# Performance work log

Hardware: AMD Instinct MI355X
Metric: run time of the kernel (lower is better)

Reference implementation:

```python
import jax, jax.numpy as jnp
import numpy as np

B, T, C, H = 4, 2048, 1024, 16
D = C // H  # head dim = 64


def _layernorm(x, g, b, eps=1e-5):
    mu = jnp.mean(x, axis=-1, keepdims=True)
    var = jnp.var(x, axis=-1, keepdims=True)
    return (x - mu) * jax.lax.rsqrt(var + eps) * g + b


def setup_inputs() -> dict:
    key = jax.random.key(0)
    ks = jax.random.split(key, 8)
    s = 0.02
    return {
        "x": jax.random.normal(ks[0], (B, T, C), dtype=jnp.float32),
        "ln1_g": jnp.ones((C,), jnp.float32),
        "ln1_b": jnp.zeros((C,), jnp.float32),
        "W_qkv": jax.random.normal(ks[1], (C, 3 * C), dtype=jnp.float32) * s,
        "b_qkv": jnp.zeros((3 * C,), jnp.float32),
        "W_o": jax.random.normal(ks[2], (C, C), dtype=jnp.float32) * s,
        "b_o": jnp.zeros((C,), jnp.float32),
        "ln2_g": jnp.ones((C,), jnp.float32),
        "ln2_b": jnp.zeros((C,), jnp.float32),
        "W_fc": jax.random.normal(ks[3], (C, 4 * C), dtype=jnp.float32) * s,
        "b_fc": jnp.zeros((4 * C,), jnp.float32),
        "W_pr": jax.random.normal(ks[4], (4 * C, C), dtype=jnp.float32) * s,
        "b_pr": jnp.zeros((C,), jnp.float32),
    }


def reference(x, ln1_g, ln1_b, W_qkv, b_qkv, W_o, b_o, ln2_g, ln2_b, W_fc, b_fc, W_pr, b_pr):
    # --- attention sub-block ---
    h = _layernorm(x, ln1_g, ln1_b)
    qkv = h @ W_qkv + b_qkv                       # [B,T,3C]
    q, k, v = jnp.split(qkv, 3, axis=-1)
    q = q.reshape(B, T, H, D).transpose(0, 2, 1, 3)  # [B,H,T,D]
    k = k.reshape(B, T, H, D).transpose(0, 2, 1, 3)
    v = v.reshape(B, T, H, D).transpose(0, 2, 1, 3)
    att = jnp.einsum("bhqd,bhkd->bhqk", q, k) * (1.0 / jnp.sqrt(jnp.float32(D)))
    causal = jnp.tril(jnp.ones((T, T), dtype=bool))
    att = jnp.where(causal, att, jnp.float32(-jnp.inf))
    att = jax.nn.softmax(att, axis=-1)
    y = jnp.einsum("bhqk,bhkd->bhqd", att, v)     # [B,H,T,D]
    y = y.transpose(0, 2, 1, 3).reshape(B, T, C)
    y = y @ W_o + b_o
    x = x + y
    # --- FFN sub-block ---
    h2 = _layernorm(x, ln2_g, ln2_b)
    f = jax.nn.gelu(h2 @ W_fc + b_fc, approximate=False)  # nn.GELU default = exact
    f = f @ W_pr + b_pr
    return x + f
```

## Files before the change

kernel.cpp:

```cpp
#include <hip/hip_runtime.h>
#include <math.h>

#define Bz 4
#define Tz 2048
#define Cz 1024
#define Hz 16
#define Dz 64
#define MTOK (Bz*Tz)

typedef __attribute__((ext_vector_type(8))) short short8;
typedef __attribute__((ext_vector_type(4))) short short4v;
typedef __attribute__((ext_vector_type(4))) float f32x4;

typedef unsigned int u32_g __attribute__((address_space(1)));
typedef unsigned int u32_l __attribute__((address_space(3)));

__device__ __forceinline__ unsigned short f2bf(float f) {
    unsigned int u = __float_as_uint(f);
    u += 0x7fffu + ((u >> 16) & 1u);
    return (unsigned short)(u >> 16);
}
__device__ __forceinline__ float bf2f(unsigned short h) {
    return __uint_as_float((unsigned int)h << 16);
}

__device__ __forceinline__ void async_cp16(const unsigned short* g, unsigned short* l) {
    __builtin_amdgcn_global_load_lds((const u32_g*)g, (u32_l*)l, 16, 0, 0);
}

__global__ void transpose_w(const float* __restrict__ W, unsigned short* __restrict__ Wt,
                            int K, int N) {
    __shared__ float tile[32][33];
    int n0 = blockIdx.x * 32, k0 = blockIdx.y * 32;
    int tx = threadIdx.x, ty = threadIdx.y;
    #pragma unroll
    for (int i = 0; i < 4; i++)
        tile[ty + i * 8][tx] = W[(size_t)(k0 + ty + i * 8) * N + n0 + tx];
    __syncthreads();
    #pragma unroll
    for (int i = 0; i < 4; i++)
        Wt[(size_t)(n0 + ty + i * 8) * K + k0 + tx] = f2bf(tile[tx][ty + i * 8]);
}

__global__ void ln_kernel(const float* __restrict__ x, const float* __restrict__ g,
                          const float* __restrict__ bb, unsigned short* __restrict__ out) {
    int tok = blockIdx.x, tid = threadIdx.x;
    const float4 v = ((const float4*)(x + (size_t)tok * Cz))[tid];
    float s = v.x + v.y + v.z + v.w;
    float sq = v.x * v.x + v.y * v.y + v.z * v.z + v.w * v.w;
    #pragma unroll
    for (int m = 1; m < 64; m <<= 1) { s += __shfl_xor(s, m); sq += __shfl_xor(sq, m); }
    __shared__ float red[8];
    int lane = tid & 63, wid = tid >> 6;
    if (!lane) { red[wid] = s; red[4 + wid] = sq; }
    __syncthreads();
    s = red[0] + red[1] + red[2] + red[3];
    sq = red[4] + red[5] + red[6] + red[7];
    float mu = s * (1.0f / Cz);
    float var = sq * (1.0f / Cz) - mu * mu;
    float rs = rsqrtf(var + 1e-5f);
    float4 gv = ((const float4*)g)[tid];
    float4 bv = ((const float4*)bb)[tid];
    short4v o;
    o[0] = f2bf((v.x - mu) * rs * gv.x + bv.x);
    o[1] = f2bf((v.y - mu) * rs * gv.y + bv.y);
    o[2] = f2bf((v.z - mu) * rs * gv.z + bv.z);
    o[3] = f2bf((v.w - mu) * rs * gv.w + bv.w);
    *(short4v*)(out + (size_t)tok * Cz + tid * 4) = o;
}

#define MODE_QKV 0
#define MODE_RESID 1
#define MODE_GELU 2

template <int MODE>
__launch_bounds__(256)
__global__ void gemm_bt(const unsigned short* __restrict__ A, const unsigned short* __restrict__ Bt,
                        int ld, int K, int N, const float* __restrict__ bias,
                        float* __restrict__ outf, unsigned short* __restrict__ outb,
                        const float* __restrict__ resid,
                        unsigned short* __restrict__ qo, unsigned short* __restrict__ ko,
                        unsigned short* __restrict__ vo) {
    __shared__ __align__(16) unsigned short As[128 * 64];
    __shared__ __align__(16) unsigned short Bs[128 * 64];
    const int tid = threadIdx.x;
    const int lane = tid & 63;
    const int quad = lane >> 4, l15 = lane & 15;
    const int wid = tid >> 6;
    const int id = blockIdx.x;
    const int m0 = ((id & 7) * 8 + ((id >> 3) & 7)) * 128;
    const int n0 = (id >> 6) * 128;
    const int wm = (wid >> 1) * 64, wn = (wid & 1) * 64;
    f32x4 acc[4][4] = {};

    const int srow = lane >> 3;
    const int scol = ((lane & 7) ^ srow) * 8;
    const unsigned short* Ag[4];
    const unsigned short* Bg[4];
    unsigned short* lA[4];
    unsigned short* lB[4];
    #pragma unroll
    for (int j = 0; j < 4; j++) {
        const int row = wid * 32 + j * 8 + srow;
        Ag[j] = A + (size_t)(m0 + row) * ld + scol;
        Bg[j] = Bt + (size_t)(n0 + row) * ld + scol;
        lA[j] = &As[(wid * 4 + j) * 512 + lane * 8];
        lB[j] = &Bs[(wid * 4 + j) * 512 + lane * 8];
    }

    for (int k0 = 0; k0 < K; k0 += 64) {
        #pragma unroll
        for (int j = 0; j < 4; j++) async_cp16(Ag[j] + k0, lA[j]);
        #pragma unroll
        for (int j = 0; j < 4; j++) async_cp16(Bg[j] + k0, lB[j]);
        __syncthreads();
        #pragma unroll
        for (int ks = 0; ks < 2; ks++) {
            short8 af[4], bfr[4];
            #pragma unroll
            for (int i = 0; i < 4; i++) {
                const int ra = wm + i * 16 + l15;
                af[i] = *(const short8*)&As[ra * 64 + (((ks << 2) + quad) ^ (ra & 7)) * 8];
            }
            #pragma unroll
            for (int i = 0; i < 4; i++) {
                const int rb = wn + i * 16 + l15;
                bfr[i] = *(const short8*)&Bs[rb * 64 + (((ks << 2) + quad) ^ (rb & 7)) * 8];
            }
            #pragma unroll
            for (int mi = 0; mi < 4; mi++)
                #pragma unroll
                for (int ni = 0; ni < 4; ni++)
                    acc[mi][ni] = __builtin_amdgcn_mfma_f32_16x16x32_bf16(af[mi], bfr[ni], acc[mi][ni], 0, 0, 0);
        }
        __syncthreads();
    }

    #pragma unroll
    for (int ni = 0; ni < 4; ni++) {
        const int col = n0 + wn + ni * 16 + l15;
        const float bv = bias[col];
        #pragma unroll
        for (int mi = 0; mi < 4; mi++) {
            #pragma unroll
            for (int r = 0; r < 4; r++) {
                const int row = m0 + wm + mi * 16 + quad * 4 + r;
                float val = acc[mi][ni][r] + bv;
                if constexpr (MODE == MODE_QKV) {
                    int which = col >> 10, cc = col & 1023;
                    int hh = cc >> 6, dd = cc & 63;
                    int b_ = row >> 11, t = row & 2047;
                    if (which == 2) {
                        vo[((size_t)(b_ * Hz + hh) * Dz + dd) * Tz + t] = f2bf(val);
                    } else {
                        unsigned short* dst = which ? ko : qo;
                        dst[((size_t)(b_ * Hz + hh) * Tz + t) * Dz + dd] = f2bf(val);
                    }
                } else if constexpr (MODE == MODE_RESID) {
                    size_t idx = (size_t)row * N + col;
                    outf[idx] = val + resid[idx];
                } else {
                    float c = val * (1.0f + 0.044715f * val * val);
                    float e = __expf(1.5957691216057308f * c);
                    float gz = val * e / (1.0f + e);
                    outb[(size_t)row * N + col] = f2bf(gz);
                }
            }
        }
    }
}

#define ATT_SC 0.18033688011112042f
__launch_bounds__(256)
__global__ void attn_kernel(const unsigned short* __restrict__ qb, const unsigned short* __restrict__ kb,
                            const unsigned short* __restrict__ vt, unsigned short* __restrict__ y) {
    __shared__ __align__(16) unsigned short Klds[64 * 64];
    __shared__ __align__(16) unsigned short Vtl[64 * 64];
    __shared__ __align__(16) unsigned short Plds[4][16 * 72];
    const int tid = threadIdx.x;
    const int lane = tid & 63, wid = tid >> 6;
    const int quad = lane >> 4, l15 = lane & 15;
    const int bh = blockIdx.x & 63;
    const int qt = 15 - (int)(blockIdx.x >> 6);
    const size_t baseT = (size_t)bh * Tz;
    const size_t vbase = (size_t)bh * Dz;
    const int qb0 = qt * 128;

    short8 qf[2][2];
    {
        const unsigned short* q0p = qb + (baseT + qb0 + wid * 16 + l15) * Dz + quad * 8;
        qf[0][0] = *(const short8*)q0p;
        qf[0][1] = *(const short8*)(q0p + 32);
        const unsigned short* q1p = q0p + (size_t)64 * Dz;
        qf[1][0] = *(const short8*)q1p;
        qf[1][1] = *(const short8*)(q1p + 32);
    }

    f32x4 o[2][4] = {};
    float lsum[2][4] = {{0.f,0.f,0.f,0.f},{0.f,0.f,0.f,0.f}};

    const int srow = lane >> 3;
    const int swz = ((lane & 7) ^ srow) * 8;
    const unsigned short* kg0 = kb + (baseT + wid * 8 + srow) * Dz + swz;
    const unsigned short* kg1 = kg0 + (size_t)32 * Dz;
    const unsigned short* vg0 = vt + (vbase + wid * 8 + srow) * Tz + swz;
    const unsigned short* vg1 = vg0 + (size_t)32 * Tz;
    unsigned short* kl0 = &Klds[wid * 512 + lane * 8];
    unsigned short* kl1 = kl0 + 2048;
    unsigned short* vl0 = &Vtl[wid * 512 + lane * 8];
    unsigned short* vl1 = vl0 + 2048;

    const int nchunk = 2 * qt + 2;

    for (int ci = 0; ci < nchunk; ci++) {
        const int k0 = ci * 64;
        async_cp16(kg0 + (size_t)k0 * Dz, kl0);
        async_cp16(kg1 + (size_t)k0 * Dz, kl1);
        async_cp16(vg0 + k0, vl0);
        async_cp16(vg1 + k0, vl1);
// ... 47 lines not shown
        __syncthreads();
    }

    const int b_ = bh >> 4, hh = bh & 15;
    #pragma unroll
    for (int t = 0; t < 2; t++)
        #pragma unroll
        for (int r = 0; r < 4; r++) {
            float ls = lsum[t][r];
            #pragma unroll
            for (int m = 1; m < 16; m <<= 1) ls += __shfl_xor(ls, m);
            float inv = 1.0f / ls;
            size_t tok = (size_t)qb0 + t * 64 + wid * 16 + quad * 4 + r;
            unsigned short* yr = y + ((size_t)b_ * Tz + tok) * Cz + hh * Dz;
            #pragma unroll
            for (int nc = 0; nc < 4; nc++)
                yr[nc * 16 + l15] = f2bf(o[t][nc][r] * inv);
        }
}

extern "C" void kernel_launch(void* const* d_in, const int* in_sizes, int n_in,
                              void* d_out, int out_size, void* d_ws, size_t ws_size,
                              hipStream_t stream) {
    const float* x    = (const float*)d_in[0];
    const float* ln1g = (const float*)d_in[1];
    const float* ln1b = (const float*)d_in[2];
    const float* Wqkv = (const float*)d_in[3];
    const float* bqkv = (const float*)d_in[4];
    const float* Wo   = (const float*)d_in[5];
    const float* bo   = (const float*)d_in[6];
    const float* ln2g = (const float*)d_in[7];
    const float* ln2b = (const float*)d_in[8];
    const float* Wfc  = (const float*)d_in[9];
    const float* bfc  = (const float*)d_in[10];
    const float* Wpr  = (const float*)d_in[11];
    const float* bpr  = (const float*)d_in[12];
    float* out = (float*)d_out;

    char* ws = (char*)d_ws;
    size_t off = 0;
    auto alloc = [&](size_t bytes) { void* p = ws + off; off += (bytes + 255) & ~(size_t)255; return p; };
    unsigned short* wqkv_t = (unsigned short*)alloc((size_t)3072 * 1024 * 2);
    unsigned short* wo_t   = (unsigned short*)alloc((size_t)1024 * 1024 * 2);
    unsigned short* wfc_t  = (unsigned short*)alloc((size_t)4096 * 1024 * 2);
    unsigned short* wpr_t  = (unsigned short*)alloc((size_t)1024 * 4096 * 2);
    unsigned short* h1     = (unsigned short*)alloc((size_t)MTOK * Cz * 2);
    unsigned short* qbuf   = (unsigned short*)alloc((size_t)MTOK * Cz * 2);
    unsigned short* kbuf   = (unsigned short*)alloc((size_t)MTOK * Cz * 2);
    unsigned short* vbuf   = (unsigned short*)alloc((size_t)MTOK * Cz * 2);
    unsigned short* ybuf   = (unsigned short*)alloc((size_t)MTOK * Cz * 2);
    float*          x1     = (float*)alloc((size_t)MTOK * Cz * 4);
    unsigned short* h2     = (unsigned short*)alloc((size_t)MTOK * Cz * 2);
    unsigned short* fbuf   = (unsigned short*)alloc((size_t)MTOK * 4096 * 2);

    dim3 tb(32, 8);
    transpose_w<<<dim3(3072 / 32, 1024 / 32), tb, 0, stream>>>(Wqkv, wqkv_t, 1024, 3072);
    transpose_w<<<dim3(1024 / 32, 1024 / 32), tb, 0, stream>>>(Wo, wo_t, 1024, 1024);
    transpose_w<<<dim3(4096 / 32, 1024 / 32), tb, 0, stream>>>(Wfc, wfc_t, 1024, 4096);
    transpose_w<<<dim3(1024 / 32, 4096 / 32), tb, 0, stream>>>(Wpr, wpr_t, 4096, 1024);

    ln_kernel<<<MTOK, 256, 0, stream>>>(x, ln1g, ln1b, h1);
    gemm_bt<MODE_QKV><<<64 * 24, 256, 0, stream>>>(h1, wqkv_t, 1024, 1024, 3072, bqkv,
                                                   nullptr, nullptr, nullptr, qbuf, kbuf, vbuf);
    attn_kernel<<<1024, 256, 0, stream>>>(qbuf, kbuf, vbuf, ybuf);
    gemm_bt<MODE_RESID><<<64 * 8, 256, 0, stream>>>(ybuf, wo_t, 1024, 1024, 1024, bo,
                                                    x1, nullptr, x, nullptr, nullptr, nullptr);
    ln_kernel<<<MTOK, 256, 0, stream>>>(x1, ln2g, ln2b, h2);
    gemm_bt<MODE_GELU><<<64 * 32, 256, 0, stream>>>(h2, wfc_t, 1024, 1024, 4096, bfc,
                                                    nullptr, fbuf, nullptr, nullptr, nullptr, nullptr);
    gemm_bt<MODE_RESID><<<64 * 8, 256, 0, stream>>>(fbuf, wpr_t, 4096, 4096, 1024, bpr,
                                                    out, nullptr, x1, nullptr, nullptr, nullptr);
}
```

Before: 530.6 us.

## Replace GEMMs with 8-wave 256-row tiles and double-buffered async LDS pipeline

Replaces the single-buffered 128x128 GEMM with two 512-thread kernels that use 256x256 or 256x128 tiles. Each K step is split into 32-wide halves, and the next tiles are prefetched with async global-to-LDS copies that overlap the MFMA work, synchronised by explicit vmcnt waits and barriers. It also adds s_setprio around the MFMA bursts. The larger tiles raise data reuse and cut LDS load overhead, but they need more registers (one block per CU) and give fewer blocks, so wave quantisation can get worse on the smaller GEMMs.

```diff
diff --git a/kernel.cpp b/kernel.cpp
--- a/kernel.cpp
+++ b/kernel.cpp
@@ -27,6 +27,10 @@
 __device__ __forceinline__ void async_cp16(const unsigned short* g, unsigned short* l) {
     __builtin_amdgcn_global_load_lds((const u32_g*)g, (u32_l*)l, 16, 0, 0);
 }
+
+#define BARX() __builtin_amdgcn_s_barrier()
+#define LGKM0() do { asm volatile("s_waitcnt lgkmcnt(0)" ::: "memory"); __builtin_amdgcn_sched_barrier(0); } while (0)
+#define VMC(n) asm volatile("s_waitcnt vmcnt(" #n ")" ::: "memory")
 
 __global__ void transpose_w(const float* __restrict__ W, unsigned short* __restrict__ Wt,
                             int K, int N) {
@@ -74,97 +78,228 @@
 #define MODE_GELU 2
 
 template <int MODE>
-__launch_bounds__(256)
-__global__ void gemm_bt(const unsigned short* __restrict__ A, const unsigned short* __restrict__ Bt,
-                        int ld, int K, int N, const float* __restrict__ bias,
-                        float* __restrict__ outf, unsigned short* __restrict__ outb,
-                        const float* __restrict__ resid,
-                        unsigned short* __restrict__ qo, unsigned short* __restrict__ ko,
-                        unsigned short* __restrict__ vo) {
-    __shared__ __align__(16) unsigned short As[128 * 64];
-    __shared__ __align__(16) unsigned short Bs[128 * 64];
+__device__ __forceinline__ void write_elem(int row, int col, float val, int N,
+                                           float* __restrict__ outf, unsigned short* __restrict__ outb,
+                                           const float* __restrict__ resid,
+                                           unsigned short* __restrict__ qo, unsigned short* __restrict__ ko,
+                                           unsigned short* __restrict__ vo) {
+    if constexpr (MODE == MODE_QKV) {
+        int which = col >> 10, cc = col & 1023;
+        int hh = cc >> 6, dd = cc & 63;
+        int b_ = row >> 11, t = row & 2047;
+        if (which == 2) {
+            vo[((size_t)(b_ * Hz + hh) * Dz + dd) * Tz + t] = f2bf(val);
+        } else {
+            unsigned short* dst = which ? ko : qo;
+            dst[((size_t)(b_ * Hz + hh) * Tz + t) * Dz + dd] = f2bf(val);
+        }
+    } else if constexpr (MODE == MODE_RESID) {
+        size_t idx = (size_t)row * N + col;
+        outf[idx] = val + resid[idx];
+    } else {
+        float c = val * (1.0f + 0.044715f * val * val);
+        float e = __expf(1.5957691216057308f * c);
+        outb[(size_t)row * N + col] = f2bf(val * e / (1.0f + e));
+    }
+}
+
+template <int MODE>
+__launch_bounds__(512, 1)
+__global__ void gemm8_n256(const unsigned short* __restrict__ A, const unsigned short* __restrict__ Bt,
+                           int lda, int K, int N, const float* __restrict__ bias,
+                           float* __restrict__ outf, unsigned short* __restrict__ outb,
+                           const float* __restrict__ resid,
+                           unsigned short* __restrict__ qo, unsigned short* __restrict__ ko,
+                           unsigned short* __restrict__ vo) {
+    __shared__ __align__(16) unsigned short As[2][2][256 * 32];
+    __shared__ __align__(16) unsigned short Bs[2][2][256 * 32];
     const int tid = threadIdx.x;
     const int lane = tid & 63;
+    const int wid = tid >> 6;
     const int quad = lane >> 4, l15 = lane & 15;
+    const int gm = wid >> 2, gn = wid & 3;
+    const int id = blockIdx.x;
+    const int rr = id >> 3;
+    const int m0 = ((id & 7) * 4 + (rr & 3)) * 256;
+    const int n0 = (rr >> 2) * 256;
+    const int NT = K >> 6;
+
+    const int srow = tid >> 2;
+    const int lseg = (tid & 3) ^ ((tid >> 3) & 3);
+    const unsigned short* Ag0 = A + (size_t)(m0 + srow) * lda + lseg * 8;
+    const unsigned short* Ag1 = A + (size_t)(m0 + 128 + srow) * lda + lseg * 8;
+    const unsigned short* Bg0 = Bt + (size_t)(n0 + srow) * lda + lseg * 8;
+    const unsigned short* Bg1 = Bt + (size_t)(n0 + 128 + srow) * lda + lseg * 8;
+
+    f32x4 acc[8][4] = {};
+    short8 af[8], bf[4];
+
+#define STA(bufd, kkd, tt) do { \
+    async_cp16(Ag0 + (size_t)(tt) * 64 + (kkd) * 32, &As[bufd][kkd][tid * 8]); \
+    async_cp16(Ag1 + (size_t)(tt) * 64 + (kkd) * 32, &As[bufd][kkd][4096 + tid * 8]); } while (0)
+#define STB(bufd, kkd, tt) do { \
+    async_cp16(Bg0 + (size_t)(tt) * 64 + (kkd) * 32, &Bs[bufd][kkd][tid * 8]); \
+    async_cp16(Bg1 + (size_t)(tt) * 64 + (kkd) * 32, &Bs[bufd][kkd][4096 + tid * 8]); } while (0)
+#define RDA(kkd) do { _Pragma("unroll") for (int mi = 0; mi < 8; mi++) { \
+    const int ra = gm * 128 + mi * 16 + l15; \
+    af[mi] = *(const short8*)&As[buf][kkd][ra * 32 + ((quad ^ ((ra >> 1) & 3)) << 3)]; } } while (0)
+#define RDB2(kkd, nia, nib) do { \
+    { const int rb = gn * 64 + (nia) * 16 + l15; \
+      bf[nia] = *(const short8*)&Bs[buf][kkd][rb * 32 + ((quad ^ ((rb >> 1) & 3)) << 3)]; } \
+    { const int rb = gn * 64 + (nib) * 16 + l15; \
+      bf[nib] = *(const short8*)&Bs[buf][kkd][rb * 32 + ((quad ^ ((rb >> 1) & 3)) << 3)]; } } while (0)
+#define MM2(nia, nib) do { _Pragma("unroll") for (int mi = 0; mi < 8; mi++) { \
+    acc[mi][nia] = __builtin_amdgcn_mfma_f32_16x16x32_bf16(af[mi], bf[nia], acc[mi][nia], 0, 0, 0); \
+    acc[mi][nib] = __builtin_amdgcn_mfma_f32_16x16x32_bf16(af[mi], bf[nib], acc[mi][nib], 0, 0, 0); } } while (0)
+
+    STA(0, 0, 0); STB(0, 0, 0);
+    STA(0, 1, 0); STB(0, 1, 0);
+    STA(1, 0, 1); STB(1, 0, 1);
+    VMC(8);
+    BARX();
+
+    for (int t = 0; t < NT; t++) {
+        const int buf = t & 1;
+        const int nb = buf ^ 1;
+        RDA(0); RDB2(0, 0, 1);
+        if (t + 1 < NT) STA(nb, 1, t + 1);
+        BARX(); LGKM0();
+        __builtin_amdgcn_s_setprio(1);
+        MM2(0, 1);
+        __builtin_amdgcn_s_setprio(0);
+        BARX();
+        RDB2(0, 2, 3);
+        if (t + 1 < NT) STB(nb, 1, t + 1);
+        BARX(); LGKM0();
+        __builtin_amdgcn_s_setprio(1);
+        MM2(2, 3);
+        __builtin_amdgcn_s_setprio(0);
+        if (t + 1 < NT) { VMC(8); } else { VMC(0); }
+        BARX();
+        RDA(1); RDB2(1, 0, 1);
+        if (t + 2 < NT) STA(buf, 0, t + 2);
+        BARX(); LGKM0();
+        __builtin_amdgcn_s_setprio(1);
+        MM2(0, 1);
+        __builtin_amdgcn_s_setprio(0);
+        BARX();
+        RDB2(1, 2, 3);
+        if (t + 2 < NT) STB(buf, 0, t + 2);
+        BARX(); LGKM0();
+        __builtin_amdgcn_s_setprio(1);
+        MM2(2, 3);
+        __builtin_amdgcn_s_setprio(0);
+        if (t + 2 < NT) { VMC(8); } else if (t + 1 < NT) { VMC(4); } else { VMC(0); }
+        BARX();
+    }
+#undef STA
+#undef STB
+#undef RDA
+#undef RDB2
+#undef MM2
+
+    #pragma unroll
+    for (int ni = 0; ni < 4; ni++) {
+        const int col = n0 + gn * 64 + ni * 16 + l15;
+        const float bv = bias[col];
+        #pragma unroll
+        for (int mi = 0; mi < 8; mi++) {
+            #pragma unroll
+            for (int r = 0; r < 4; r++) {
+                const int row = m0 + gm * 128 + mi * 16 + quad * 4 + r;
+                write_elem<MODE>(row, col, acc[mi][ni][r] + bv, N, outf, outb, resid, qo, ko, vo);
+            }
+        }
+    }
+}
+
+template <int MODE>
+__launch_bounds__(512, 1)
+__global__ void gemm8_n128(const unsigned short* __restrict__ A, const unsigned short* __restrict__ Bt,
+                           int lda, int K, int N, const float* __restrict__ bias,
+                           float* __restrict__ outf, unsigned short* __restrict__ outb,
+                           const float* __restrict__ resid,
+                           unsigned short* __restrict__ qo, unsigned short* __restrict__ ko,
+                           unsigned short* __restrict__ vo) {
+    __shared__ __align__(16) unsigned short As[2][2][256 * 32];
+    __shared__ __align__(16) unsigned short Bs[2][2][128 * 32];
+    const int tid = threadIdx.x;
+    const int lane = tid & 63;
     const int wid = tid >> 6;
+    const int quad = lane >> 4, l15 = lane & 15;
+    const int gm = wid >> 1, gn = wid & 1;
     const int id = blockIdx.x;
-    const int m0 = ((id & 7) * 8 + ((id >> 3) & 7)) * 128;
-    const int n0 = (id >> 6) * 128;
-    const int wm = (wid >> 1) * 64, wn = (wid & 1) * 64;
+    const int rr = id >> 3;
+    const int m0 = ((id & 7) * 4 + (rr & 3)) * 256;
+    const int n0 = (rr >> 2) * 128;
+    const int NT = K >> 6;
+
+    const int srow = tid >> 2;
+    const int lseg = (tid & 3) ^ ((tid >> 3) & 3);
+    const unsigned short* Ag0 = A + (size_t)(m0 + srow) * lda + lseg * 8;
+    const unsigned short* Ag1 = A + (size_t)(m0 + 128 + srow) * lda + lseg * 8;
+    const unsigned short* Bg0 = Bt + (size_t)(n0 + srow) * lda + lseg * 8;
+
     f32x4 acc[4][4] = {};
-
-    const int srow = lane >> 3;
-    const int scol = ((lane & 7) ^ srow) * 8;
-    const unsigned short* Ag[4];
-    const unsigned short* Bg[4];
-    unsigned short* lA[4];
-    unsigned short* lB[4];
-    #pragma unroll
-    for (int j = 0; j < 4; j++) {
-        const int row = wid * 32 + j * 8 + srow;
-        Ag[j] = A + (size_t)(m0 + row) * ld + scol;
-        Bg[j] = Bt + (size_t)(n0 + row) * ld + scol;
-        lA[j] = &As[(wid * 4 + j) * 512 + lane * 8];
-        lB[j] = &Bs[(wid * 4 + j) * 512 + lane * 8];
-    }
-
-    for (int k0 = 0; k0 < K; k0 += 64) {
-        #pragma unroll
-        for (int j = 0; j < 4; j++) async_cp16(Ag[j] + k0, lA[j]);
-        #pragma unroll
-        for (int j = 0; j < 4; j++) async_cp16(Bg[j] + k0, lB[j]);
-        __syncthreads();
-        #pragma unroll
-        for (int ks = 0; ks < 2; ks++) {
-            short8 af[4], bfr[4];
-            #pragma unroll
-            for (int i = 0; i < 4; i++) {
-                const int ra = wm + i * 16 + l15;
-                af[i] = *(const short8*)&As[ra * 64 + (((ks << 2) + quad) ^ (ra & 7)) * 8];
-            }
-            #pragma unroll
-            for (int i = 0; i < 4; i++) {
-                const int rb = wn + i * 16 + l15;
-                bfr[i] = *(const short8*)&Bs[rb * 64 + (((ks << 2) + quad) ^ (rb & 7)) * 8];
-            }
-            #pragma unroll
-            for (int mi = 0; mi < 4; mi++)
-                #pragma unroll
-                for (int ni = 0; ni < 4; ni++)
-                    acc[mi][ni] = __builtin_amdgcn_mfma_f32_16x16x32_bf16(af[mi], bfr[ni], acc[mi][ni], 0, 0, 0);
-        }
-        __syncthreads();
-    }
+    short8 af[4], bf[4];
+
+#define STA(bufd, kkd, tt) do { \
+    async_cp16(Ag0 + (size_t)(tt) * 64 + (kkd) * 32, &As[bufd][kkd][tid * 8]); \
+    async_cp16(Ag1 + (size_t)(tt) * 64 + (kkd) * 32, &As[bufd][kkd][4096 + tid * 8]); } while (0)
+#define STB(bufd, kkd, tt) \
+    async_cp16(Bg0 + (size_t)(tt) * 64 + (kkd) * 32, &Bs[bufd][kkd][tid * 8])
+#define RDA(kkd) do { _Pragma("unroll") for (int mi = 0; mi < 4; mi++) { \
+    const int ra = gm * 64 + mi * 16 + l15; \
+    af[mi] = *(const short8*)&As[buf][kkd][ra * 32 + ((quad ^ ((ra >> 1) & 3)) << 3)]; } } while (0)
+#define RDB(kkd) do { _Pragma("unroll") for (int ni = 0; ni < 4; ni++) { \
+    const int rb = gn * 64 + ni * 16 + l15; \
+    bf[ni] = *(const short8*)&Bs[buf][kkd][rb * 32 + ((quad ^ ((rb >> 1) & 3)) << 3)]; } } while (0)
+#define MM16() do { _Pragma("unroll") for (int mi = 0; mi < 4; mi++) \
+    _Pragma("unroll") for (int ni = 0; ni < 4; ni++) \
+        acc[mi][ni] = __builtin_amdgcn_mfma_f32_16x16x32_bf16(af[mi], bf[ni], acc[mi][ni], 0, 0, 0); } while (0)
+
+    STA(0, 0, 0); STB(0, 0, 0);
+    STA(0, 1, 0); STB(0, 1, 0);
+    STA(1, 0, 1); STB(1, 0, 1);
+    VMC(6);
+    BARX();
+
+    for (int t = 0; t < NT; t++) {
+        const int buf = t & 1;
+        const int nb = buf ^ 1;
+        RDA(0); RDB(0);
+        if (t + 1 < NT) { STA(nb, 1, t + 1); STB(nb, 1, t + 1); }
+        BARX(); LGKM0();
+        __builtin_amdgcn_s_setprio(1);
+        MM16();
+        __builtin_amdgcn_s_setprio(0);
+        if (t + 1 < NT) { VMC(6); } else { VMC(0); }
+        BARX();
+        RDA(1); RDB(1);
+        if (t + 2 < NT) { STA(buf, 0, t + 2); STB(buf, 0, t + 2); }
+        BARX(); LGKM0();
+        __builtin_amdgcn_s_setprio(1);
+        MM16();
+        __builtin_amdgcn_s_setprio(0);
+        if (t + 2 < NT) { VMC(6); } else if (t + 1 < NT) { VMC(3); } else { VMC(0); }
+        BARX();
+    }
+#undef STA
+#undef STB
+#undef RDA
+#undef RDB
+#undef MM16
 
     #pragma unroll
     for (int ni = 0; ni < 4; ni++) {
-        const int col = n0 + wn + ni * 16 + l15;
+        const int col = n0 + gn * 64 + ni * 16 + l15;
         const float bv = bias[col];
         #pragma unroll
         for (int mi = 0; mi < 4; mi++) {
             #pragma unroll
             for (int r = 0; r < 4; r++) {
-                const int row = m0 + wm + mi * 16 + quad * 4 + r;
-                float val = acc[mi][ni][r] + bv;
-                if constexpr (MODE == MODE_QKV) {
-                    int which = col >> 10, cc = col & 1023;
-                    int hh = cc >> 6, dd = cc & 63;
-                    int b_ = row >> 11, t = row & 2047;
-                    if (which == 2) {
-                        vo[((size_t)(b_ * Hz + hh) * Dz + dd) * Tz + t] = f2bf(val);
-                    } else {
-                        unsigned short* dst = which ? ko : qo;
-                        dst[((size_t)(b_ * Hz + hh) * Tz + t) * Dz + dd] = f2bf(val);
-                    }
-                } else if constexpr (MODE == MODE_RESID) {
-                    size_t idx = (size_t)row * N + col;
-                    outf[idx] = val + resid[idx];
-                } else {
-                    float c = val * (1.0f + 0.044715f * val * val);
-                    float e = __expf(1.5957691216057308f * c);
-                    float gz = val * e / (1.0f + e);
-                    outb[(size_t)row * N + col] = f2bf(gz);
-                }
+                const int row = m0 + gm * 64 + mi * 16 + quad * 4 + r;
+                write_elem<MODE>(row, col, acc[mi][ni][r] + bv, N, outf, outb, resid, qo, ko, vo);
             }
         }
     }
@@ -326,14 +461,14 @@
     transpose_w<<<dim3(1024 / 32, 4096 / 32), tb, 0, stream>>>(Wpr, wpr_t, 4096, 1024);
 
     ln_kernel<<<MTOK, 256, 0, stream>>>(x, ln1g, ln1b, h1);
-    gemm_bt<MODE_QKV><<<64 * 24, 256, 0, stream>>>(h1, wqkv_t, 1024, 1024, 3072, bqkv,
-                                                   nullptr, nullptr, nullptr, qbuf, kbuf, vbuf);
+    gemm8_n256<MODE_QKV><<<384, 512, 0, stream>>>(h1, wqkv_t, 1024, 1024, 3072, bqkv,
+                                                  nullptr, nullptr, nullptr, qbuf, kbuf, vbuf);
     attn_kernel<<<1024, 256, 0, stream>>>(qbuf, kbuf, vbuf, ybuf);
-    gemm_bt<MODE_RESID><<<64 * 8, 256, 0, stream>>>(ybuf, wo_t, 1024, 1024, 1024, bo,
+    gemm8_n128<MODE_RESID><<<256, 512, 0, stream>>>(ybuf, wo_t, 1024, 1024, 1024, bo,
                                                     x1, nullptr, x, nullptr, nullptr, nullptr);
     ln_kernel<<<MTOK, 256, 0, stream>>>(x1, ln2g, ln2b, h2);
-    gemm_bt<MODE_GELU><<<64 * 32, 256, 0, stream>>>(h2, wfc_t, 1024, 1024, 4096, bfc,
-                                                    nullptr, fbuf, nullptr, nullptr, nullptr, nullptr);
-    gemm_bt<MODE_RESID><<<64 * 8, 256, 0, stream>>>(fbuf, wpr_t, 4096, 4096, 1024, bpr,
+    gemm8_n256<MODE_GELU><<<512, 512, 0, stream>>>(h2, wfc_t, 1024, 1024, 4096, bfc,
+                                                   nullptr, fbuf, nullptr, nullptr, nullptr, nullptr);
+    gemm8_n128<MODE_RESID><<<256, 512, 0, stream>>>(fbuf, wpr_t, 4096, 4096, 1024, bpr,
                                                     out, nullptr, x1, nullptr, nullptr, nullptr);
 }
```

After: 564.7 us. +6.4%, slower.

## Replace GEMM with triple-buffered 512-thread kernels and separate V transpose

Applied to the files above, without the earlier changes.

Replaces the single-buffered 128x128 GEMM with two 512-thread kernels: 256x128 tiles for QKV/out-proj/down-proj and 256x256 tiles for the FC layer. Both use a K=32 three-stage async global-to-LDS pipeline with vmcnt waits and one barrier per step, plus MFMA priority raising. The QKV epilogue now writes V in row layout to a scratch buffer aliasing fbuf, and a new transpose_v kernel produces the transposed V, replacing the scattered strided stores. This aims to hide load latency and improve reuse, at the cost of an extra kernel launch and a larger register/LDS footprint that limits occupancy to one block per CU.

```diff
diff --git a/kernel.cpp b/kernel.cpp
--- a/kernel.cpp
+++ b/kernel.cpp
@@ -28,6 +28,9 @@
     __builtin_amdgcn_global_load_lds((const u32_g*)g, (u32_l*)l, 16, 0, 0);
 }
 
+#define BARX() __builtin_amdgcn_s_barrier()
+#define VMCM(n) asm volatile("s_waitcnt vmcnt(" #n ")" ::: "memory")
+
 __global__ void transpose_w(const float* __restrict__ W, unsigned short* __restrict__ Wt,
                             int K, int N) {
     __shared__ float tile[32][33];
@@ -40,6 +43,30 @@
     #pragma unroll
     for (int i = 0; i < 4; i++)
         Wt[(size_t)(n0 + ty + i * 8) * K + k0 + tx] = f2bf(tile[tx][ty + i * 8]);
+}
+
+__global__ void transpose_v(const unsigned short* __restrict__ in, unsigned short* __restrict__ out) {
+    __shared__ unsigned short tile[64][68];
+    const int bh = blockIdx.x;
+    const int t0 = blockIdx.y * 64;
+    const int tid = threadIdx.x;
+    const int r4 = tid >> 4;
+    const int c4 = tid & 15;
+    #pragma unroll
+    for (int p = 0; p < 4; p++) {
+        const int r = p * 16 + r4;
+        *(short4v*)&tile[r][c4 * 4] =
+            *(const short4v*)&in[((size_t)bh * Tz + t0 + r) * Dz + c4 * 4];
+    }
+    __syncthreads();
+    #pragma unroll
+    for (int p = 0; p < 4; p++) {
+        const int d = p * 16 + r4;
+        short4v o;
+        #pragma unroll
+        for (int j = 0; j < 4; j++) o[j] = tile[c4 * 4 + j][d];
+        *(short4v*)&out[((size_t)bh * Dz + d) * Tz + t0 + c4 * 4] = o;
+    }
 }
 
 __global__ void ln_kernel(const float* __restrict__ x, const float* __restrict__ g,
@@ -74,97 +101,204 @@
 #define MODE_GELU 2
 
 template <int MODE>
-__launch_bounds__(256)
-__global__ void gemm_bt(const unsigned short* __restrict__ A, const unsigned short* __restrict__ Bt,
-                        int ld, int K, int N, const float* __restrict__ bias,
-                        float* __restrict__ outf, unsigned short* __restrict__ outb,
-                        const float* __restrict__ resid,
-                        unsigned short* __restrict__ qo, unsigned short* __restrict__ ko,
-                        unsigned short* __restrict__ vo) {
-    __shared__ __align__(16) unsigned short As[128 * 64];
-    __shared__ __align__(16) unsigned short Bs[128 * 64];
+__device__ __forceinline__ void write_elem(int row, int col, float val, int N,
+                                           float* __restrict__ outf, unsigned short* __restrict__ outb,
+                                           const float* __restrict__ resid,
+                                           unsigned short* __restrict__ qo, unsigned short* __restrict__ ko,
+                                           unsigned short* __restrict__ vo) {
+    if constexpr (MODE == MODE_QKV) {
+        int which = col >> 10, cc = col & 1023;
+        int hh = cc >> 6, dd = cc & 63;
+        int b_ = row >> 11, t = row & 2047;
+        unsigned short* dst = (which == 0) ? qo : (which == 1) ? ko : vo;
+        dst[((size_t)(b_ * Hz + hh) * Tz + t) * Dz + dd] = f2bf(val);
+    } else if constexpr (MODE == MODE_RESID) {
+        size_t idx = (size_t)row * N + col;
+        outf[idx] = val + resid[idx];
+    } else {
+        float c = val * (1.0f + 0.044715f * val * val);
+        float e = __expf(1.5957691216057308f * c);
+        outb[(size_t)row * N + col] = f2bf(val * e / (1.0f + e));
+    }
+}
+
+template <int MODE>
+__launch_bounds__(512, 1)
+__global__ void gemm3_n256(const unsigned short* __restrict__ A, const unsigned short* __restrict__ Bt,
+                           int lda, int K, int N, const float* __restrict__ bias,
+                           float* __restrict__ outf, unsigned short* __restrict__ outb,
+                           const float* __restrict__ resid,
+                           unsigned short* __restrict__ qo, unsigned short* __restrict__ ko,
+                           unsigned short* __restrict__ vo) {
+    __shared__ __align__(16) unsigned short LDS[3 * 16384];
     const int tid = threadIdx.x;
     const int lane = tid & 63;
+    const int wid = tid >> 6;
     const int quad = lane >> 4, l15 = lane & 15;
+    const int gm = wid >> 2, gn = wid & 3;
+    const int id = blockIdx.x;
+    const int rr = id >> 3;
+    const int m0 = ((id & 7) * 4 + (rr & 3)) * 256;
+    const int n0 = (rr >> 2) * 256;
+    const int NT = K >> 5;
+
+    const int lseg = (tid & 3) ^ ((tid >> 3) & 3);
+    const int srow = tid >> 2;
+    const unsigned short* Ag0 = A + (size_t)(m0 + srow) * lda + lseg * 8;
+    const unsigned short* Ag1 = A + (size_t)(m0 + 128 + srow) * lda + lseg * 8;
+    const unsigned short* Bg0 = Bt + (size_t)(n0 + srow) * lda + lseg * 8;
+    const unsigned short* Bg1 = Bt + (size_t)(n0 + 128 + srow) * lda + lseg * 8;
+
+    unsigned short* sl0 = LDS;
+    unsigned short* sl1 = LDS + 16384;
+    unsigned short* sl2 = LDS + 32768;
+
+    int offA[8], offB[4];
+    #pragma unroll
+    for (int mi = 0; mi < 8; mi++) {
+        const int ra = gm * 128 + mi * 16 + l15;
+        offA[mi] = ra * 32 + ((quad ^ ((ra >> 1) & 3)) << 3);
+    }
+    #pragma unroll
+    for (int ni = 0; ni < 4; ni++) {
+        const int rb = gn * 64 + ni * 16 + l15;
+        offB[ni] = 8192 + rb * 32 + ((quad ^ ((rb >> 1) & 3)) << 3);
+    }
+
+    f32x4 acc[8][4] = {};
+
+#define STAGE(sp, tt) do { \
+    const size_t kof = (size_t)(tt) * 32; \
+    async_cp16(Ag0 + kof, (sp) + tid * 8); \
+    async_cp16(Ag1 + kof, (sp) + 4096 + tid * 8); \
+    async_cp16(Bg0 + kof, (sp) + 8192 + tid * 8); \
+    async_cp16(Bg1 + kof, (sp) + 12288 + tid * 8); } while (0)
+#define COMPUTE(sp) do { \
+    short8 af[8], bf[4]; \
+    _Pragma("unroll") for (int mi = 0; mi < 8; mi++) af[mi] = *(const short8*)((sp) + offA[mi]); \
+    _Pragma("unroll") for (int ni = 0; ni < 4; ni++) bf[ni] = *(const short8*)((sp) + offB[ni]); \
+    __builtin_amdgcn_s_setprio(1); \
+    _Pragma("unroll") for (int mi = 0; mi < 8; mi++) \
+        _Pragma("unroll") for (int ni = 0; ni < 4; ni++) \
+            acc[mi][ni] = __builtin_amdgcn_mfma_f32_16x16x32_bf16(af[mi], bf[ni], acc[mi][ni], 0, 0, 0); \
+    __builtin_amdgcn_s_setprio(0); } while (0)
+
+    STAGE(sl0, 0);
+    STAGE(sl1, 1);
+
+    for (int t = 0; t < NT - 1; t++) {
+        VMCM(4);
+        BARX();
+        if (t + 2 < NT) STAGE(sl2, t + 2);
+        COMPUTE(sl0);
+        unsigned short* tmp = sl0; sl0 = sl1; sl1 = sl2; sl2 = tmp;
+    }
+    VMCM(0);
+    BARX();
+    COMPUTE(sl0);
+#undef STAGE
+#undef COMPUTE
+
+    #pragma unroll
+    for (int ni = 0; ni < 4; ni++) {
+        const int col = n0 + gn * 64 + ni * 16 + l15;
+        const float bv = bias[col];
+        #pragma unroll
+        for (int mi = 0; mi < 8; mi++) {
+            #pragma unroll
+            for (int r = 0; r < 4; r++) {
+                const int row = m0 + gm * 128 + mi * 16 + quad * 4 + r;
+                write_elem<MODE>(row, col, acc[mi][ni][r] + bv, N, outf, outb, resid, qo, ko, vo);
+            }
+        }
+    }
+}
+
+template <int MODE>
+__launch_bounds__(512, 1)
+__global__ void gemm3_n128(const unsigned short* __restrict__ A, const unsigned short* __restrict__ Bt,
+                           int lda, int K, int N, const float* __restrict__ bias,
+                           float* __restrict__ outf, unsigned short* __restrict__ outb,
+                           const float* __restrict__ resid,
+                           unsigned short* __restrict__ qo, unsigned short* __restrict__ ko,
+                           unsigned short* __restrict__ vo) {
+    __shared__ __align__(16) unsigned short LDS[3 * 12288];
+    const int tid = threadIdx.x;
+    const int lane = tid & 63;
     const int wid = tid >> 6;
+    const int quad = lane >> 4, l15 = lane & 15;
+    const int gm = wid >> 1, gn = wid & 1;
     const int id = blockIdx.x;
-    const int m0 = ((id & 7) * 8 + ((id >> 3) & 7)) * 128;
-    const int n0 = (id >> 6) * 128;
-    const int wm = (wid >> 1) * 64, wn = (wid & 1) * 64;
+    const int rr = id >> 3;
+    const int m0 = ((id & 7) * 4 + (rr & 3)) * 256;
+    const int n0 = (rr >> 2) * 128;
+    const int NT = K >> 5;
+
+    const int lseg = (tid & 3) ^ ((tid >> 3) & 3);
+    const int srow = tid >> 2;
+    const unsigned short* Ag0 = A + (size_t)(m0 + srow) * lda + lseg * 8;
+    const unsigned short* Ag1 = A + (size_t)(m0 + 128 + srow) * lda + lseg * 8;
+    const unsigned short* Bg0 = Bt + (size_t)(n0 + srow) * lda + lseg * 8;
+
+    unsigned short* sl0 = LDS;
+    unsigned short* sl1 = LDS + 12288;
+    unsigned short* sl2 = LDS + 24576;
+
+    int offA[4], offB[4];
+    #pragma unroll
+    for (int mi = 0; mi < 4; mi++) {
+        const int ra = gm * 64 + mi * 16 + l15;
+        offA[mi] = ra * 32 + ((quad ^ ((ra >> 1) & 3)) << 3);
+    }
+    #pragma unroll
+    for (int ni = 0; ni < 4; ni++) {
+        const int rb = gn * 64 + ni * 16 + l15;
+        offB[ni] = 8192 + rb * 32 + ((quad ^ ((rb >> 1) & 3)) << 3);
+    }
+
     f32x4 acc[4][4] = {};
 
-    const int srow = lane >> 3;
-    const int scol = ((lane & 7) ^ srow) * 8;
-    const unsigned short* Ag[4];
-    const unsigned short* Bg[4];
-    unsigned short* lA[4];
-    unsigned short* lB[4];
-    #pragma unroll
-    for (int j = 0; j < 4; j++) {
-        const int row = wid * 32 + j * 8 + srow;
-        Ag[j] = A + (size_t)(m0 + row) * ld + scol;
-        Bg[j] = Bt + (size_t)(n0 + row) * ld + scol;
-        lA[j] = &As[(wid * 4 + j) * 512 + lane * 8];
-        lB[j] = &Bs[(wid * 4 + j) * 512 + lane * 8];
-    }
-
-    for (int k0 = 0; k0 < K; k0 += 64) {
-        #pragma unroll
-        for (int j = 0; j < 4; j++) async_cp16(Ag[j] + k0, lA[j]);
-        #pragma unroll
-        for (int j = 0; j < 4; j++) async_cp16(Bg[j] + k0, lB[j]);
-        __syncthreads();
-        #pragma unroll
-        for (int ks = 0; ks < 2; ks++) {
-            short8 af[4], bfr[4];
-            #pragma unroll
-            for (int i = 0; i < 4; i++) {
-                const int ra = wm + i * 16 + l15;
-                af[i] = *(const short8*)&As[ra * 64 + (((ks << 2) + quad) ^ (ra & 7)) * 8];
-            }
-            #pragma unroll
-            for (int i = 0; i < 4; i++) {
-                const int rb = wn + i * 16 + l15;
-                bfr[i] = *(const short8*)&Bs[rb * 64 + (((ks << 2) + quad) ^ (rb & 7)) * 8];
-            }
-            #pragma unroll
-            for (int mi = 0; mi < 4; mi++)
-                #pragma unroll
-                for (int ni = 0; ni < 4; ni++)
-                    acc[mi][ni] = __builtin_amdgcn_mfma_f32_16x16x32_bf16(af[mi], bfr[ni], acc[mi][ni], 0, 0, 0);
-        }
-        __syncthreads();
-    }
+#define STAGE(sp, tt) do { \
+    const size_t kof = (size_t)(tt) * 32; \
+    async_cp16(Ag0 + kof, (sp) + tid * 8); \
+    async_cp16(Ag1 + kof, (sp) + 4096 + tid * 8); \
+    async_cp16(Bg0 + kof, (sp) + 8192 + tid * 8); } while (0)
+#define COMPUTE(sp) do { \
+    short8 af[4], bf[4]; \
+    _Pragma("unroll") for (int mi = 0; mi < 4; mi++) af[mi] = *(const short8*)((sp) + offA[mi]); \
+    _Pragma("unroll") for (int ni = 0; ni < 4; ni++) bf[ni] = *(const short8*)((sp) + offB[ni]); \
+    __builtin_amdgcn_s_setprio(1); \
+    _Pragma("unroll") for (int mi = 0; mi < 4; mi++) \
+        _Pragma("unroll") for (int ni = 0; ni < 4; ni++) \
+            acc[mi][ni] = __builtin_amdgcn_mfma_f32_16x16x32_bf16(af[mi], bf[ni], acc[mi][ni], 0, 0, 0); \
+    __builtin_amdgcn_s_setprio(0); } while (0)
+
+    STAGE(sl0, 0);
+    STAGE(sl1, 1);
+
+    for (int t = 0; t < NT - 1; t++) {
+        VMCM(3);
+        BARX();
+        if (t + 2 < NT) STAGE(sl2, t + 2);
+        COMPUTE(sl0);
+        unsigned short* tmp = sl0; sl0 = sl1; sl1 = sl2; sl2 = tmp;
+    }
+    VMCM(0);
+    BARX();
+    COMPUTE(sl0);
+#undef STAGE
+#undef COMPUTE
 
     #pragma unroll
     for (int ni = 0; ni < 4; ni++) {
-        const int col = n0 + wn + ni * 16 + l15;
+        const int col = n0 + gn * 64 + ni * 16 + l15;
         const float bv = bias[col];
         #pragma unroll
         for (int mi = 0; mi < 4; mi++) {
             #pragma unroll
             for (int r = 0; r < 4; r++) {
-                const int row = m0 + wm + mi * 16 + quad * 4 + r;
-                float val = acc[mi][ni][r] + bv;
-                if constexpr (MODE == MODE_QKV) {
-                    int which = col >> 10, cc = col & 1023;
-                    int hh = cc >> 6, dd = cc & 63;
-                    int b_ = row >> 11, t = row & 2047;
-                    if (which == 2) {
-                        vo[((size_t)(b_ * Hz + hh) * Dz + dd) * Tz + t] = f2bf(val);
-                    } else {
-                        unsigned short* dst = which ? ko : qo;
-                        dst[((size_t)(b_ * Hz + hh) * Tz + t) * Dz + dd] = f2bf(val);
-                    }
-                } else if constexpr (MODE == MODE_RESID) {
-                    size_t idx = (size_t)row * N + col;
-                    outf[idx] = val + resid[idx];
-                } else {
-                    float c = val * (1.0f + 0.044715f * val * val);
-                    float e = __expf(1.5957691216057308f * c);
-                    float gz = val * e / (1.0f + e);
-                    outb[(size_t)row * N + col] = f2bf(gz);
-                }
+                const int row = m0 + gm * 64 + mi * 16 + quad * 4 + r;
+                write_elem<MODE>(row, col, acc[mi][ni][r] + bv, N, outf, outb, resid, qo, ko, vo);
             }
         }
     }
@@ -318,6 +452,7 @@
     float*          x1     = (float*)alloc((size_t)MTOK * Cz * 4);
     unsigned short* h2     = (unsigned short*)alloc((size_t)MTOK * Cz * 2);
     unsigned short* fbuf   = (unsigned short*)alloc((size_t)MTOK * 4096 * 2);
+    unsigned short* vtmp   = fbuf;
 
     dim3 tb(32, 8);
     transpose_w<<<dim3(3072 / 32, 1024 / 32), tb, 0, stream>>>(Wqkv, wqkv_t, 1024, 3072);
@@ -326,14 +461,15 @@
     transpose_w<<<dim3(1024 / 32, 4096 / 32), tb, 0, stream>>>(Wpr, wpr_t, 4096, 1024);
 
     ln_kernel<<<MTOK, 256, 0, stream>>>(x, ln1g, ln1b, h1);
-    gemm_bt<MODE_QKV><<<64 * 24, 256, 0, stream>>>(h1, wqkv_t, 1024, 1024, 3072, bqkv,
-                                                   nullptr, nullptr, nullptr, qbuf, kbuf, vbuf);
+    gemm3_n128<MODE_QKV><<<768, 512, 0, stream>>>(h1, wqkv_t, 1024, 1024, 3072, bqkv,
+                                                  nullptr, nullptr, nullptr, qbuf, kbuf, vtmp);
+    transpose_v<<<dim3(64, 32), 256, 0, stream>>>(vtmp, vbuf);
     attn_kernel<<<1024, 256, 0, stream>>>(qbuf, kbuf, vbuf, ybuf);
-    gemm_bt<MODE_RESID><<<64 * 8, 256, 0, stream>>>(ybuf, wo_t, 1024, 1024, 1024, bo,
+    gemm3_n128<MODE_RESID><<<256, 512, 0, stream>>>(ybuf, wo_t, 1024, 1024, 1024, bo,
                                                     x1, nullptr, x, nullptr, nullptr, nullptr);
     ln_kernel<<<MTOK, 256, 0, stream>>>(x1, ln2g, ln2b, h2);
-    gemm_bt<MODE_GELU><<<64 * 32, 256, 0, stream>>>(h2, wfc_t, 1024, 1024, 4096, bfc,
-                                                    nullptr, fbuf, nullptr, nullptr, nullptr, nullptr);
-    gemm_bt<MODE_RESID><<<64 * 8, 256, 0, stream>>>(fbuf, wpr_t, 4096, 4096, 1024, bpr,
+    gemm3_n256<MODE_GELU><<<512, 512, 0, stream>>>(h2, wfc_t, 1024, 1024, 4096, bfc,
+                                                   nullptr, fbuf, nullptr, nullptr, nullptr, nullptr);
+    gemm3_n128<MODE_RESID><<<256, 512, 0, stream>>>(fbuf, wpr_t, 4096, 4096, 1024, bpr,
                                                     out, nullptr, x1, nullptr, nullptr, nullptr);
 }
```

Result: faster. 514.9 us (-3.0%).

## Replace GEMM with 4-stage async-LDS pipelined 256x128 tile kernel and separate V transpose

Applied to the files above, without the earlier changes.

Rewrites the bf16 GEMM into a 512-thread kernel with 256x128 output tiles and a 4-deep ring of K=32 LDS stages. The stages are fed by global_load_lds with vmcnt waits, double-buffered register fragments and setprio around the MFMA bursts, so loads overlap compute instead of a sync per K-step. The QKV epilogue now writes V in row layout into scratch (aliasing fbuf), and a new transpose_v kernel produces the transposed V layout that attention expects. This replaces the strided scattered V stores with coalesced ones. The cost is an extra kernel launch and pass over V, plus single-block occupancy at 512 threads.

```diff
diff --git a/kernel.cpp b/kernel.cpp
--- a/kernel.cpp
+++ b/kernel.cpp
@@ -28,6 +28,9 @@
     __builtin_amdgcn_global_load_lds((const u32_g*)g, (u32_l*)l, 16, 0, 0);
 }
 
+#define BARX() __builtin_amdgcn_s_barrier()
+#define VMCM(n) asm volatile("s_waitcnt vmcnt(" #n ")" ::: "memory")
+
 __global__ void transpose_w(const float* __restrict__ W, unsigned short* __restrict__ Wt,
                             int K, int N) {
     __shared__ float tile[32][33];
@@ -40,6 +43,30 @@
     #pragma unroll
     for (int i = 0; i < 4; i++)
         Wt[(size_t)(n0 + ty + i * 8) * K + k0 + tx] = f2bf(tile[tx][ty + i * 8]);
+}
+
+__global__ void transpose_v(const unsigned short* __restrict__ in, unsigned short* __restrict__ out) {
+    __shared__ unsigned short tile[64][68];
+    const int bh = blockIdx.x;
+    const int t0 = blockIdx.y * 64;
+    const int tid = threadIdx.x;
+    const int r4 = tid >> 4;
+    const int c4 = tid & 15;
+    #pragma unroll
+    for (int p = 0; p < 4; p++) {
+        const int r = p * 16 + r4;
+        *(short4v*)&tile[r][c4 * 4] =
+            *(const short4v*)&in[((size_t)bh * Tz + t0 + r) * Dz + c4 * 4];
+    }
+    __syncthreads();
+    #pragma unroll
+    for (int p = 0; p < 4; p++) {
+        const int d = p * 16 + r4;
+        short4v o;
+        #pragma unroll
+        for (int j = 0; j < 4; j++) o[j] = tile[c4 * 4 + j][d];
+        *(short4v*)&out[((size_t)bh * Dz + d) * Tz + t0 + c4 * 4] = o;
+    }
 }
 
 __global__ void ln_kernel(const float* __restrict__ x, const float* __restrict__ g,
@@ -74,96 +101,133 @@
 #define MODE_GELU 2
 
 template <int MODE>
-__launch_bounds__(256)
-__global__ void gemm_bt(const unsigned short* __restrict__ A, const unsigned short* __restrict__ Bt,
-                        int ld, int K, int N, const float* __restrict__ bias,
-                        float* __restrict__ outf, unsigned short* __restrict__ outb,
-                        const float* __restrict__ resid,
-                        unsigned short* __restrict__ qo, unsigned short* __restrict__ ko,
-                        unsigned short* __restrict__ vo) {
-    __shared__ __align__(16) unsigned short As[128 * 64];
-    __shared__ __align__(16) unsigned short Bs[128 * 64];
+__launch_bounds__(512, 1)
+__global__ void gemm_p(const unsigned short* __restrict__ A, const unsigned short* __restrict__ Bt,
+                       int lda, int K, int N, const float* __restrict__ bias,
+                       float* __restrict__ outf, unsigned short* __restrict__ outb,
+                       const float* __restrict__ resid,
+                       unsigned short* __restrict__ qo, unsigned short* __restrict__ ko,
+                       unsigned short* __restrict__ vo) {
+    __shared__ __align__(16) unsigned short LDS[4 * 12288];
     const int tid = threadIdx.x;
     const int lane = tid & 63;
+    const int wid = tid >> 6;
     const int quad = lane >> 4, l15 = lane & 15;
-    const int wid = tid >> 6;
+    const int gm = wid >> 1, gn = wid & 1;
     const int id = blockIdx.x;
-    const int m0 = ((id & 7) * 8 + ((id >> 3) & 7)) * 128;
-    const int n0 = (id >> 6) * 128;
-    const int wm = (wid >> 1) * 64, wn = (wid & 1) * 64;
+    const int rr = id >> 3;
+    const int m0 = ((id & 7) * 4 + (rr & 3)) * 256;
+    const int n0 = (rr >> 2) * 128;
+    const int NT = K >> 5;
+
+    const int lseg = (tid & 3) ^ ((tid >> 3) & 3);
+    const int srow = tid >> 2;
+    const unsigned short* Ag0 = A + (size_t)(m0 + srow) * lda + lseg * 8;
+    const unsigned short* Ag1 = A + (size_t)(m0 + 128 + srow) * lda + lseg * 8;
+    const unsigned short* Bg0 = Bt + (size_t)(n0 + srow) * lda + lseg * 8;
+
+    int offA[4], offB[4];
+    #pragma unroll
+    for (int mi = 0; mi < 4; mi++) {
+        const int ra = gm * 64 + mi * 16 + l15;
+        offA[mi] = ra * 32 + ((quad ^ ((ra >> 1) & 3)) << 3);
+    }
+    #pragma unroll
+    for (int ni = 0; ni < 4; ni++) {
+        const int rb = gn * 64 + ni * 16 + l15;
+        offB[ni] = 8192 + rb * 32 + ((quad ^ ((rb >> 1) & 3)) << 3);
+    }
+
     f32x4 acc[4][4] = {};
-
-    const int srow = lane >> 3;
-    const int scol = ((lane & 7) ^ srow) * 8;
-    const unsigned short* Ag[4];
-    const unsigned short* Bg[4];
-    unsigned short* lA[4];
-    unsigned short* lB[4];
-    #pragma unroll
-    for (int j = 0; j < 4; j++) {
-        const int row = wid * 32 + j * 8 + srow;
-        Ag[j] = A + (size_t)(m0 + row) * ld + scol;
-        Bg[j] = Bt + (size_t)(n0 + row) * ld + scol;
-        lA[j] = &As[(wid * 4 + j) * 512 + lane * 8];
-        lB[j] = &Bs[(wid * 4 + j) * 512 + lane * 8];
-    }
-
-    for (int k0 = 0; k0 < K; k0 += 64) {
-        #pragma unroll
-        for (int j = 0; j < 4; j++) async_cp16(Ag[j] + k0, lA[j]);
-        #pragma unroll
-        for (int j = 0; j < 4; j++) async_cp16(Bg[j] + k0, lB[j]);
-        __syncthreads();
-        #pragma unroll
-        for (int ks = 0; ks < 2; ks++) {
-            short8 af[4], bfr[4];
-            #pragma unroll
-            for (int i = 0; i < 4; i++) {
-                const int ra = wm + i * 16 + l15;
-                af[i] = *(const short8*)&As[ra * 64 + (((ks << 2) + quad) ^ (ra & 7)) * 8];
-            }
-            #pragma unroll
-            for (int i = 0; i < 4; i++) {
-                const int rb = wn + i * 16 + l15;
-                bfr[i] = *(const short8*)&Bs[rb * 64 + (((ks << 2) + quad) ^ (rb & 7)) * 8];
-            }
-            #pragma unroll
-            for (int mi = 0; mi < 4; mi++)
+    short8 afA[4], bfA[4], afB[4], bfB[4];
+
+#define STG(tt) do { \
+    unsigned short* sp_ = LDS + (((unsigned)(tt)) & 3u) * 12288; \
+    const size_t kof_ = (size_t)(tt) * 32; \
+    async_cp16(Ag0 + kof_, sp_ + tid * 8); \
+    async_cp16(Ag1 + kof_, sp_ + 4096 + tid * 8); \
+    async_cp16(Bg0 + kof_, sp_ + 8192 + tid * 8); } while (0)
+#define RDS(afX, bfX, tt) do { \
+    const unsigned short* sp_ = LDS + (((unsigned)(tt)) & 3u) * 12288; \
+    _Pragma("unroll") for (int mi = 0; mi < 4; mi++) afX[mi] = *(const short8*)(sp_ + offA[mi]); \
+    _Pragma("unroll") for (int ni = 0; ni < 4; ni++) bfX[ni] = *(const short8*)(sp_ + offB[ni]); } while (0)
+#define MMS(afX, bfX) do { \
+    __builtin_amdgcn_s_setprio(1); \
+    _Pragma("unroll") for (int mi = 0; mi < 4; mi++) \
+        _Pragma("unroll") for (int ni = 0; ni < 4; ni++) \
+            acc[mi][ni] = __builtin_amdgcn_mfma_f32_16x16x32_bf16(afX[mi], bfX[ni], acc[mi][ni], 0, 0, 0); \
+    __builtin_amdgcn_s_setprio(0); } while (0)
+
+    STG(0); STG(1); STG(2);
+    VMCM(6);
+    BARX();
+    RDS(afA, bfA, 0);
+
+    for (int t = 0; t < NT; t += 2) {
+        if (t + 2 < NT) { VMCM(3); } else { VMCM(0); }
+        BARX();
+        if (t + 3 < NT) STG(t + 3);
+        RDS(afB, bfB, t + 1);
+        MMS(afA, bfA);
+        if (t + 2 < NT) { VMCM(3); }
+        BARX();
+        if (t + 4 < NT) STG(t + 4);
+        if (t + 2 < NT) RDS(afA, bfA, t + 2);
+        MMS(afB, bfB);
+    }
+#undef STG
+#undef RDS
+#undef MMS
+
+    float bv[4];
+    #pragma unroll
+    for (int ni = 0; ni < 4; ni++) bv[ni] = bias[n0 + gn * 64 + ni * 16 + l15];
+
+    if constexpr (MODE == MODE_QKV) {
+        const int colb = n0 + gn * 64;
+        const int which = colb >> 10;
+        const int hh = (colb & 1023) >> 6;
+        unsigned short* dst = (which == 0) ? qo : (which == 1) ? ko : vo;
+        #pragma unroll
+        for (int mi = 0; mi < 4; mi++) {
+            #pragma unroll
+            for (int r = 0; r < 4; r++) {
+                const int row = m0 + gm * 64 + mi * 16 + quad * 4 + r;
+                const int b_ = row >> 11, tt = row & 2047;
+                unsigned short* rp = dst + ((size_t)(b_ * Hz + hh) * Tz + tt) * Dz;
                 #pragma unroll
                 for (int ni = 0; ni < 4; ni++)
-                    acc[mi][ni] = __builtin_amdgcn_mfma_f32_16x16x32_bf16(af[mi], bfr[ni], acc[mi][ni], 0, 0, 0);
+                    rp[ni * 16 + l15] = f2bf(acc[mi][ni][r] + bv[ni]);
+            }
         }
-        __syncthreads();
-    }
-
-    #pragma unroll
-    for (int ni = 0; ni < 4; ni++) {
-        const int col = n0 + wn + ni * 16 + l15;
-        const float bv = bias[col];
+    } else if constexpr (MODE == MODE_RESID) {
         #pragma unroll
         for (int mi = 0; mi < 4; mi++) {
             #pragma unroll
             for (int r = 0; r < 4; r++) {
-                const int row = m0 + wm + mi * 16 + quad * 4 + r;
-                float val = acc[mi][ni][r] + bv;
-                if constexpr (MODE == MODE_QKV) {
-                    int which = col >> 10, cc = col & 1023;
-                    int hh = cc >> 6, dd = cc & 63;
-                    int b_ = row >> 11, t = row & 2047;
-                    if (which == 2) {
-                        vo[((size_t)(b_ * Hz + hh) * Dz + dd) * Tz + t] = f2bf(val);
-                    } else {
-                        unsigned short* dst = which ? ko : qo;
-                        dst[((size_t)(b_ * Hz + hh) * Tz + t) * Dz + dd] = f2bf(val);
-                    }
-                } else if constexpr (MODE == MODE_RESID) {
-                    size_t idx = (size_t)row * N + col;
-                    outf[idx] = val + resid[idx];
-                } else {
+                const int row = m0 + gm * 64 + mi * 16 + quad * 4 + r;
+                float* rp = outf + (size_t)row * N + n0 + gn * 64;
+                const float* rr_ = resid + (size_t)row * N + n0 + gn * 64;
+                #pragma unroll
+                for (int ni = 0; ni < 4; ni++) {
+                    const int c = ni * 16 + l15;
+                    rp[c] = acc[mi][ni][r] + bv[ni] + rr_[c];
+                }
+            }
+        }
+    } else {
+        #pragma unroll
+        for (int mi = 0; mi < 4; mi++) {
+            #pragma unroll
+            for (int r = 0; r < 4; r++) {
+                const int row = m0 + gm * 64 + mi * 16 + quad * 4 + r;
+                unsigned short* rp = outb + (size_t)row * N + n0 + gn * 64;
+                #pragma unroll
+                for (int ni = 0; ni < 4; ni++) {
+                    float val = acc[mi][ni][r] + bv[ni];
                     float c = val * (1.0f + 0.044715f * val * val);
                     float e = __expf(1.5957691216057308f * c);
-                    float gz = val * e / (1.0f + e);
-                    outb[(size_t)row * N + col] = f2bf(gz);
+                    rp[ni * 16 + l15] = f2bf(val * e / (1.0f + e));
                 }
             }
         }
@@ -318,6 +382,7 @@
     float*          x1     = (float*)alloc((size_t)MTOK * Cz * 4);
     unsigned short* h2     = (unsigned short*)alloc((size_t)MTOK * Cz * 2);
     unsigned short* fbuf   = (unsigned short*)alloc((size_t)MTOK * 4096 * 2);
+    unsigned short* vtmp   = fbuf;
 
     dim3 tb(32, 8);
     transpose_w<<<dim3(3072 / 32, 1024 / 32), tb, 0, stream>>>(Wqkv, wqkv_t, 1024, 3072);
@@ -326,14 +391,15 @@
     transpose_w<<<dim3(1024 / 32, 4096 / 32), tb, 0, stream>>>(Wpr, wpr_t, 4096, 1024);
 
     ln_kernel<<<MTOK, 256, 0, stream>>>(x, ln1g, ln1b, h1);
-    gemm_bt<MODE_QKV><<<64 * 24, 256, 0, stream>>>(h1, wqkv_t, 1024, 1024, 3072, bqkv,
-                                                   nullptr, nullptr, nullptr, qbuf, kbuf, vbuf);
+    gemm_p<MODE_QKV><<<768, 512, 0, stream>>>(h1, wqkv_t, 1024, 1024, 3072, bqkv,
+                                              nullptr, nullptr, nullptr, qbuf, kbuf, vtmp);
+    transpose_v<<<dim3(64, 32), 256, 0, stream>>>(vtmp, vbuf);
     attn_kernel<<<1024, 256, 0, stream>>>(qbuf, kbuf, vbuf, ybuf);
-    gemm_bt<MODE_RESID><<<64 * 8, 256, 0, stream>>>(ybuf, wo_t, 1024, 1024, 1024, bo,
-                                                    x1, nullptr, x, nullptr, nullptr, nullptr);
+    gemm_p<MODE_RESID><<<256, 512, 0, stream>>>(ybuf, wo_t, 1024, 1024, 1024, bo,
+                                                x1, nullptr, x, nullptr, nullptr, nullptr);
     ln_kernel<<<MTOK, 256, 0, stream>>>(x1, ln2g, ln2b, h2);
-    gemm_bt<MODE_GELU><<<64 * 32, 256, 0, stream>>>(h2, wfc_t, 1024, 1024, 4096, bfc,
-                                                    nullptr, fbuf, nullptr, nullptr, nullptr, nullptr);
-    gemm_bt<MODE_RESID><<<64 * 8, 256, 0, stream>>>(fbuf, wpr_t, 4096, 4096, 1024, bpr,
-                                                    out, nullptr, x1, nullptr, nullptr, nullptr);
-}
+    gemm_p<MODE_GELU><<<1024, 512, 0, stream>>>(h2, wfc_t, 1024, 1024, 4096, bfc,
+                                                nullptr, fbuf, nullptr, nullptr, nullptr, nullptr);
+    gemm_p<MODE_RESID><<<256, 512, 0, stream>>>(fbuf, wpr_t, 4096, 4096, 1024, bpr,
+                                                out, nullptr, x1, nullptr, nullptr, nullptr);
+}
```

Measured after the change: 517.8 us. 1.02x faster.
